# Kernel optimization log

Hardware: AMD Instinct MI355X
Metric: run time of the kernel (lower is better)

The kernel has to match this reference:

```python
import jax, jax.numpy as jnp
import numpy as np
import math

# batch, seq_len, emb_ch, convlru_hidden_ch, spatial H, W (W must equal H, see diag_embed broadcast)
B, L, E, C, H, W = 4, 32, 64, 96, 32, 32


def setup_inputs():
    key = jax.random.key(0)
    ks = jax.random.split(key, 24)
    r_min, r_max = 0.8, 0.99
    u1 = jax.random.uniform(ks[0], (C, H))
    u2 = jax.random.uniform(ks[1], (C, H))
    nu_log = jnp.log(-0.5 * jnp.log(u1 * (r_max ** 2 - r_min ** 2) + r_min ** 2))
    theta_log = jnp.log(u2 * 2.0 * np.pi)
    lam_abs = jnp.exp(-jnp.exp(nu_log))  # |lambda| = exp(-nu)
    gamma_log = jnp.log(jnp.sqrt(1.0 - lam_abs ** 2))
    params_log = jnp.vstack([nu_log, theta_log, gamma_log]).astype(jnp.float32)

    def w(k, shape, fan_in):
        s = 1.0 / np.sqrt(fan_in)
        return jax.random.uniform(k, shape, minval=-s, maxval=s, dtype=jnp.float32)

    return {
        "x": jax.random.normal(ks[2], (B, L, E, H, W), jnp.float32),
        "mask": jnp.ones((B, L), jnp.float32),
        "params_log": params_log,
        "Wb_r": w(ks[3], (C, E), E), "Wb_i": w(ks[4], (C, E), E),
        "bb_r": w(ks[5], (C,), E), "bb_i": w(ks[6], (C,), E),
        "Wp1_r": w(ks[7], (C, C), C), "Wp1_i": w(ks[8], (C, C), C),
        "bp1_r": w(ks[9], (C,), C), "bp1_i": w(ks[10], (C,), C),
        "Wp2_r": w(ks[11], (C, C), C), "Wp2_i": w(ks[12], (C, C), C),
        "bp2_r": w(ks[13], (C,), C), "bp2_i": w(ks[14], (C,), C),
        "Wc_r": w(ks[15], (E, C), C), "Wc_i": w(ks[16], (E, C), C),
        "bc_r": w(ks[17], (E,), C), "bc_i": w(ks[18], (E,), C),
        "ln_w": jnp.ones((E, H, W), jnp.float32),
        "ln_b": jnp.zeros((E, H, W), jnp.float32),
    }


def _forward(x, mask, params_log, Wb, bb, Wp1, bp1, Wp2, bp2, Wc, bc, ln_w, ln_b):
    nu, theta, gamma = jnp.split(jnp.exp(params_log), 3, axis=0)  # each (C, H)
    lamb = jnp.exp(jnp.complex64(-nu + 1j * theta))               # (C, H)
    xc = x.astype(jnp.complex64)
    # proj_B: 1x1 complex conv == channel einsum
    h = jnp.einsum('blehw,ce->blchw', xc, Wb) + bb[:, None, None]
    h = jnp.fft.fft2(h)  # over last two axes
    h = jnp.einsum('blkhw,ck->blchw', h, Wp1) + bp1[:, None, None]
    eye = jnp.eye(H, dtype=jnp.float32)  # (H, W); requires W == H
    # h * torch.diag_embed(gamma): elementwise mult with a diagonal (C,H,H) matrix
    # -> zeroes off-diagonal spatial entries (faithful to the torch code)
    h = h * (gamma[:, :, None] * eye)
    m = jnp.broadcast_to(mask[:, :, None, None, None], h.shape).astype(jnp.float32)
    log2L = int(math.ceil(math.log2(L)))
    lamb = lamb[None]  # (1, C, H)
    for i in range(1, log2L + 1):
        l = 2 ** i
        if i > 1:
            lamb = jnp.concatenate([lamb, lamb * lamb[-1]], axis=0)  # (l//2, C, H)
        hr = h.reshape(B * L // l, l, C, H, W)
        mr = m.reshape(B * L // l, l, C, H, W)
        h1, h2 = hr[:, : l // 2], hr[:, l // 2:]
        # term[n,j,c,a,b] = lamb[j,c,a] * eye[a,b] * h1[n,-1,c,a,b] * mask[n,l//2-1,c,a,b]
        term = (lamb[None, :, :, :, None] * eye) * h1[:, -1:] * mr[:, l // 2 - 1: l // 2]
        h = jnp.concatenate([h1, h2 + term], axis=1).reshape(B, L, C, H, W)
    h = jnp.fft.ifft2(h)
    h = jnp.einsum('blkhw,ck->blchw', h, Wp2) + bp2[:, None, None]
    h = jnp.einsum('blchw,ec->blehw', h, Wc) + bc[:, None, None]
    h = h.real
    # dropout is identity in eval mode
    mu = jnp.mean(h, axis=(-3, -2, -1), keepdims=True)
    var = jnp.var(h, axis=(-3, -2, -1), keepdims=True)
    h = (h - mu) / jnp.sqrt(var + 1e-5) * ln_w + ln_b
    return h + x


def reference(x, mask, params_log, Wb_r, Wb_i, bb_r, bb_i, Wp1_r, Wp1_i, bp1_r, bp1_i, Wp2_r, Wp2_i, bp2_r, bp2_i, Wc_r, Wc_i, bc_r, bc_i, ln_w, ln_b):
    cx = lambda r, i: (r + 1j * i).astype(jnp.complex64)
    return _forward(x, mask, params_log,
                    cx(Wb_r, Wb_i), cx(bb_r, bb_i),
                    cx(Wp1_r, Wp1_i), cx(bp1_r, bp1_i),
                    cx(Wp2_r, Wp2_i), cx(bp2_r, bp2_i),
                    cx(Wc_r, Wc_i), cx(bc_r, bc_i),
                    ln_w, ln_b)
```

## Files before the change

kernel.cpp:

```cpp
#include <hip/hip_runtime.h>

static constexpr int BL = 128;
static constexpr int OFF_COS  = 0;
static constexpr int OFF_SIN  = 1024;
static constexpr int OFF_ARE  = 2048;
static constexpr int OFF_AIM  = 8192;
static constexpr int OFF_WRE  = 14336;
static constexpr int OFF_WIM  = 20480;
static constexpr int OFF_LRE  = 26624;
static constexpr int OFF_LIM  = 29696;
static constexpr int OFF_GAM  = 32768;
static constexpr int OFF_BH0R = 35840;
static constexpr int OFF_BH0I = 35936;
static constexpr int OFF_BRR  = 36032;
static constexpr int OFF_QF   = 36096;
static constexpr int OFF_Y    = 560384;
static constexpr int OFF_V    = 1346816;
static constexpr int OFF_R    = 1871104;
static constexpr int OFF_ST   = 2133248;

__global__ __launch_bounds__(256) void k0_precompute(
    const float* __restrict__ params_log,
    const float* __restrict__ Wb_r, const float* __restrict__ Wb_i,
    const float* __restrict__ bb_r, const float* __restrict__ bb_i,
    const float* __restrict__ Wp1_r, const float* __restrict__ Wp1_i,
    const float* __restrict__ Wp2_r, const float* __restrict__ Wp2_i,
    const float* __restrict__ Wc_r, const float* __restrict__ Wc_i,
    const float* __restrict__ bp2_r, const float* __restrict__ bp2_i,
    const float* __restrict__ bc_r, float* __restrict__ ws) {
  int tid = blockIdx.x * 256 + threadIdx.x;
  if (tid < 1024) {
    int h = tid >> 5, s = tid & 31;
    int m = (h * s) & 31;
    float ang = (float)m * 0.19634954084936207f;
    ws[OFF_COS + tid] = cosf(ang);
    ws[OFF_SIN + tid] = sinf(ang);
  } else if (tid < 4096) {
    int i = tid - 1024;
    float nu = expf(params_log[i]);
    float th = expf(params_log[3072 + i]);
    float g  = expf(params_log[6144 + i]);
    float rr = expf(-nu);
    ws[OFF_LRE + i] = rr * cosf(th);
    ws[OFF_LIM + i] = rr * sinf(th);
    ws[OFF_GAM + i] = g;
  } else if (tid < 10240) {
    int i = tid - 4096;
    int c = i >> 6, e = i & 63;
    float are = 0.f, aim = 0.f;
    for (int k = 0; k < 96; ++k) {
      float pr = Wp1_r[c * 96 + k], pi = Wp1_i[c * 96 + k];
      float wr = Wb_r[k * 64 + e], wi = Wb_i[k * 64 + e];
      are += pr * wr - pi * wi;
      aim += pr * wi + pi * wr;
    }
    ws[OFF_ARE + i] = are;
    ws[OFF_AIM + i] = aim;
  } else if (tid < 16384) {
    int i = tid - 10240;
    int e = i / 96, c = i - e * 96;
    float are = 0.f, aim = 0.f;
    for (int k = 0; k < 96; ++k) {
      float wr = Wc_r[e * 96 + k], wi = Wc_i[e * 96 + k];
      float pr = Wp2_r[k * 96 + c], pi = Wp2_i[k * 96 + c];
      are += wr * pr - wi * pi;
      aim += wr * pi + wi * pr;
    }
    ws[OFF_WRE + i] = are;
    ws[OFF_WIM + i] = aim;
  } else if (tid < 16480) {
    int c = tid - 16384;
    float re = 0.f, im = 0.f;
    for (int k = 0; k < 96; ++k) {
      float pr = Wp1_r[c * 96 + k], pi = Wp1_i[c * 96 + k];
      float br = bb_r[k], bi = bb_i[k];
      re += pr * br - pi * bi;
      im += pr * bi + pi * br;
    }
    ws[OFF_BH0R + c] = 1024.f * re;
    ws[OFF_BH0I + c] = 1024.f * im;
  } else if (tid < 16544) {
    int e = tid - 16480;
    float re = 0.f;
    for (int k = 0; k < 96; ++k)
      re += Wc_r[e * 96 + k] * bp2_r[k] - Wc_i[e * 96 + k] * bp2_i[k];
    ws[OFF_BRR + e] = re + bc_r[e];
  }
}

__global__ __launch_bounds__(256) void k1_qdft(const float* __restrict__ x,
                                               float* __restrict__ ws) {
  __shared__ float pl[4][1024];
  __shared__ float qsh[4][32];
  int wave = threadIdx.x >> 6, lane = threadIdx.x & 63;
  int plane = blockIdx.x * 4 + wave;
  const float* xp = x + (size_t)plane * 1024;
#pragma unroll
  for (int j = 0; j < 16; ++j) pl[wave][j * 64 + lane] = xp[j * 64 + lane];
  __syncthreads();
  int s = lane & 31, half = lane >> 5;
  float acc = 0.f;
#pragma unroll
  for (int u0 = 0; u0 < 16; ++u0) {
    int u = half * 16 + u0;
    acc += pl[wave][u * 32 + ((s - u) & 31)];
  }
  acc += __shfl_xor(acc, 32);
  if (lane < 32) qsh[wave][lane] = acc;
  __syncthreads();
  int h = lane & 31;
  const float* Ft = ws + (lane < 32 ? OFF_COS : OFF_SIN);
  float sum = 0.f;
#pragma unroll
  for (int s2 = 0; s2 < 32; ++s2) sum += qsh[wave][s2] * Ft[s2 * 32 + h];
  if (lane >= 32) sum = -sum;
  ws[OFF_QF + plane * 64 + h * 2 + (lane < 32 ? 0 : 1)] = sum;
}

__global__ __launch_bounds__(256) void k2_mix1(float* __restrict__ ws,
                                               const float* __restrict__ bp1_r,
                                               const float* __restrict__ bp1_i) {
  __shared__ float qre[64][32], qim[64][32];
  int bl = blockIdx.x / 12, chunk = blockIdx.x % 12;
  const float2* qF = (const float2*)(ws + OFF_QF) + bl * 2048;
  for (int i = threadIdx.x; i < 2048; i += 256) {
    float2 v = qF[i];
    qre[i >> 5][i & 31] = v.x;
    qim[i >> 5][i & 31] = v.y;
  }
  __syncthreads();
  int c = chunk * 8 + (threadIdx.x >> 5), h = threadIdx.x & 31;
  const float* Ar = ws + OFF_ARE + c * 64;
  const float* Ai = ws + OFF_AIM + c * 64;
  float re = 0.f, im = 0.f;
#pragma unroll 8
  for (int e = 0; e < 64; ++e) {
    float ar = Ar[e], ai = Ai[e], qr = qre[e][h], qi = qim[e][h];
    re += ar * qr - ai * qi;
    im += ar * qi + ai * qr;
  }
  if (h == 0) { re += ws[OFF_BH0R + c]; im += ws[OFF_BH0I + c]; }
  re += bp1_r[c];
  im += bp1_i[c];
  float g = ws[OFF_GAM + c * 32 + h];
  ((float2*)(ws + OFF_Y))[(bl * 96 + c) * 32 + h] = make_float2(g * re, g * im);
}

__global__ __launch_bounds__(256) void k3_scan(float* __restrict__ ws,
                                               const float* __restrict__ mask) {
  int tid = blockIdx.x * 256 + threadIdx.x;
  int b = tid / 3072, r = tid - b * 3072;
  float lr = ws[OFF_LRE + r], li = ws[OFF_LIM + r];
  float2* Y = (float2*)(ws + OFF_Y) + (size_t)b * 32 * 3072 + r;
  float2 v = Y[0];
  float sr = v.x, si = v.y;
  for (int l = 1; l < 32; ++l) {
    float m = mask[b * 32 + l - 1];
    float cr = m * (lr * sr - li * si);
    float ci = m * (lr * si + li * sr);
    v = Y[l * 3072];
    sr = v.x + cr;
    si = v.y + ci;
    Y[l * 3072] = make_float2(sr, si);
  }
}

__global__ __launch_bounds__(256) void k4_mix2(float* __restrict__ ws) {
  __shared__ float sre[96][32], sim_[96][32];
  int bl = blockIdx.x >> 3, chunk = blockIdx.x & 7;
  const float2* S = (const float2*)(ws + OFF_Y) + bl * 3072;
  for (int i = threadIdx.x; i < 3072; i += 256) {
    float2 v = S[i];
    sre[i >> 5][i & 31] = v.x;
    sim_[i >> 5][i & 31] = v.y;
  }
  __syncthreads();
  int e = chunk * 8 + (threadIdx.x >> 5), h = threadIdx.x & 31;
  const float* Wr = ws + OFF_WRE + e * 96;
  const float* Wi = ws + OFF_WIM + e * 96;
  float re = 0.f, im = 0.f;
#pragma unroll 8
  for (int c = 0; c < 96; ++c) {
    float wr = Wr[c], wi = Wi[c], a = sre[c][h], b2 = sim_[c][h];
    re += wr * a - wi * b2;
    im += wr * b2 + wi * a;
  }
  ((float2*)(ws + OFF_V))[(bl * 64 + e) * 32 + h] = make_float2(re, im);
}

__global__ __launch_bounds__(256) void k5a_post(float* __restrict__ ws) {
  __shared__ float vre[64][32], vim[64][32];
  __shared__ float red[8];
  int bl = blockIdx.x;
  const float2* V = (const float2*)(ws + OFF_V) + bl * 2048;
  for (int i = threadIdx.x; i < 2048; i += 256) {
    float2 v = V[i];
    vre[i >> 5][i & 31] = v.x;
    vim[i >> 5][i & 31] = v.y;
  }
  __syncthreads();
  float sum = 0.f, sumsq = 0.f;
  float* R = ws + OFF_R + bl * 2048;
  for (int i = threadIdx.x; i < 2048; i += 256) {
    int e = i >> 5, s = i & 31;
    float acc = 0.f;
#pragma unroll
    for (int h = 0; h < 32; ++h)
      acc += vre[e][h] * ws[OFF_COS + h * 32 + s] - vim[e][h] * ws[OFF_SIN + h * 32 + s];
    float r = acc * (1.0f / 1024.0f) + ws[OFF_BRR + e];
    R[i] = r;
    sum += r;
    sumsq += r * r;
  }
#pragma unroll
  for (int off = 32; off > 0; off >>= 1) {
    sum += __shfl_down(sum, off);
    sumsq += __shfl_down(sumsq, off);
  }
  int wave = threadIdx.x >> 6, lane = threadIdx.x & 63;
  if (lane == 0) { red[wave] = sum; red[4 + wave] = sumsq; }
  __syncthreads();
  if (threadIdx.x == 0) {
    float s0 = red[0] + red[1] + red[2] + red[3];
    float q0 = red[4] + red[5] + red[6] + red[7];
    float mu = s0 * (1.0f / 2048.0f);
    float var = q0 * (1.0f / 2048.0f) - mu * mu;
    ws[OFF_ST + bl * 2] = mu;
    ws[OFF_ST + bl * 2 + 1] = rsqrtf(var + 1e-5f);
  }
}

__global__ __launch_bounds__(256) void k5b_final(const float* __restrict__ x,
                                                 const float* __restrict__ lnw,
                                                 const float* __restrict__ lnb,
                                                 const float* __restrict__ ws,
                                                 float* __restrict__ out) {
  int gid = blockIdx.x * 256 + threadIdx.x;
  int flat = gid * 4;
  int bl = flat >> 16;
  int rem = flat & 65535;
  int e = rem >> 10;
  int pos = rem & 1023;
  int u = pos >> 5, v = pos & 31;
  float mu = ws[OFF_ST + bl * 2], istd = ws[OFF_ST + bl * 2 + 1];
  const float* Rrow = ws + OFF_R + bl * 2048 + e * 32;
  const float4 xin = ((const float4*)x)[gid];
  const float4 lw = ((const float4*)lnw)[rem >> 2];
  const float4 lb = ((const float4*)lnb)[rem >> 2];
  float4 o;
  o.x = (Rrow[(u + v) & 31] - mu) * istd * lw.x + lb.x + xin.x;
  o.y = (Rrow[(u + v + 1) & 31] - mu) * istd * lw.y + lb.y + xin.y;
  o.z = (Rrow[(u + v + 2) & 31] - mu) * istd * lw.z + lb.z + xin.z;
  o.w = (Rrow[(u + v + 3) & 31] - mu) * istd * lw.w + lb.w + xin.w;
  ((float4*)out)[gid] = o;
}

extern "C" void kernel_launch(void* const* d_in, const int* in_sizes, int n_in,
                              void* d_out, int out_size, void* d_ws, size_t ws_size,
                              hipStream_t stream) {
  const float* x          = (const float*)d_in[0];
  const float* mask       = (const float*)d_in[1];
  const float* params_log = (const float*)d_in[2];
  const float* Wb_r  = (const float*)d_in[3];
  const float* Wb_i  = (const float*)d_in[4];
  const float* bb_r  = (const float*)d_in[5];
  const float* bb_i  = (const float*)d_in[6];
  const float* Wp1_r = (const float*)d_in[7];
  const float* Wp1_i = (const float*)d_in[8];
  const float* bp1_r = (const float*)d_in[9];
  const float* bp1_i = (const float*)d_in[10];
  const float* Wp2_r = (const float*)d_in[11];
  const float* Wp2_i = (const float*)d_in[12];
  const float* bp2_r = (const float*)d_in[13];
  const float* bp2_i = (const float*)d_in[14];
  const float* Wc_r  = (const float*)d_in[15];
  const float* Wc_i  = (const float*)d_in[16];
  const float* bc_r  = (const float*)d_in[17];
  const float* ln_w  = (const float*)d_in[19];
  const float* ln_b  = (const float*)d_in[20];
  float* ws  = (float*)d_ws;
  float* out = (float*)d_out;

  k0_precompute<<<65, 256, 0, stream>>>(params_log, Wb_r, Wb_i, bb_r, bb_i,
                                        Wp1_r, Wp1_i, Wp2_r, Wp2_i, Wc_r, Wc_i,
                                        bp2_r, bp2_i, bc_r, ws);
  k1_qdft<<<2048, 256, 0, stream>>>(x, ws);
  k2_mix1<<<1536, 256, 0, stream>>>(ws, bp1_r, bp1_i);
  k3_scan<<<48, 256, 0, stream>>>(ws, mask);
  k4_mix2<<<1024, 256, 0, stream>>>(ws);
  k5a_post<<<128, 256, 0, stream>>>(ws);
  k5b_final<<<8192, 256, 0, stream>>>(x, ln_w, ln_b, ws, out);
}
```

Measured before the change: 177.3 us.

## Fuse kernels: merge precompute with DFT, mix2 with post, restructure scan

Merges the weight precompute into the spatial DFT kernel as extra blocks, and fuses the output channel mix with the inverse DFT and LayerNorm partial statistics. This cuts the pipeline from seven launches to five and drops the V intermediate. The scan now runs 64-thread blocks that load all 32 timesteps into registers before the recurrence, and the twiddle tables come from a 32-entry in-LDS sincos table instead of global tables. The final kernel stages one R row in shared memory and combines the two partial statistics, at the cost of more register pressure in the scan and the fused mix kernel.

```diff
diff --git a/kernel.cpp b/kernel.cpp
--- a/kernel.cpp
+++ b/kernel.cpp
@@ -15,11 +15,11 @@
 static constexpr int OFF_BRR  = 36032;
 static constexpr int OFF_QF   = 36096;
 static constexpr int OFF_Y    = 560384;
-static constexpr int OFF_V    = 1346816;
 static constexpr int OFF_R    = 1871104;
 static constexpr int OFF_ST   = 2133248;
 
-__global__ __launch_bounds__(256) void k0_precompute(
+__global__ __launch_bounds__(256) void kA(
+    const float* __restrict__ x,
     const float* __restrict__ params_log,
     const float* __restrict__ Wb_r, const float* __restrict__ Wb_i,
     const float* __restrict__ bb_r, const float* __restrict__ bb_i,
@@ -28,106 +28,107 @@
     const float* __restrict__ Wc_r, const float* __restrict__ Wc_i,
     const float* __restrict__ bp2_r, const float* __restrict__ bp2_i,
     const float* __restrict__ bc_r, float* __restrict__ ws) {
-  int tid = blockIdx.x * 256 + threadIdx.x;
-  if (tid < 1024) {
-    int h = tid >> 5, s = tid & 31;
-    int m = (h * s) & 31;
-    float ang = (float)m * 0.19634954084936207f;
-    ws[OFF_COS + tid] = cosf(ang);
-    ws[OFF_SIN + tid] = sinf(ang);
-  } else if (tid < 4096) {
-    int i = tid - 1024;
-    float nu = expf(params_log[i]);
-    float th = expf(params_log[3072 + i]);
-    float g  = expf(params_log[6144 + i]);
-    float rr = expf(-nu);
-    ws[OFF_LRE + i] = rr * cosf(th);
-    ws[OFF_LIM + i] = rr * sinf(th);
-    ws[OFF_GAM + i] = g;
-  } else if (tid < 10240) {
-    int i = tid - 4096;
-    int c = i >> 6, e = i & 63;
-    float are = 0.f, aim = 0.f;
-    for (int k = 0; k < 96; ++k) {
-      float pr = Wp1_r[c * 96 + k], pi = Wp1_i[c * 96 + k];
-      float wr = Wb_r[k * 64 + e], wi = Wb_i[k * 64 + e];
-      are += pr * wr - pi * wi;
-      aim += pr * wi + pi * wr;
-    }
-    ws[OFF_ARE + i] = are;
-    ws[OFF_AIM + i] = aim;
-  } else if (tid < 16384) {
-    int i = tid - 10240;
-    int e = i / 96, c = i - e * 96;
-    float are = 0.f, aim = 0.f;
-    for (int k = 0; k < 96; ++k) {
-      float wr = Wc_r[e * 96 + k], wi = Wc_i[e * 96 + k];
-      float pr = Wp2_r[k * 96 + c], pi = Wp2_i[k * 96 + c];
-      are += wr * pr - wi * pi;
-      aim += wr * pi + wi * pr;
-    }
-    ws[OFF_WRE + i] = are;
-    ws[OFF_WIM + i] = aim;
-  } else if (tid < 16480) {
-    int c = tid - 16384;
-    float re = 0.f, im = 0.f;
-    for (int k = 0; k < 96; ++k) {
-      float pr = Wp1_r[c * 96 + k], pi = Wp1_i[c * 96 + k];
-      float br = bb_r[k], bi = bb_i[k];
-      re += pr * br - pi * bi;
-      im += pr * bi + pi * br;
-    }
-    ws[OFF_BH0R + c] = 1024.f * re;
-    ws[OFF_BH0I + c] = 1024.f * im;
-  } else if (tid < 16544) {
-    int e = tid - 16480;
-    float re = 0.f;
-    for (int k = 0; k < 96; ++k)
-      re += Wc_r[e * 96 + k] * bp2_r[k] - Wc_i[e * 96 + k] * bp2_i[k];
-    ws[OFF_BRR + e] = re + bc_r[e];
-  }
-}
-
-__global__ __launch_bounds__(256) void k1_qdft(const float* __restrict__ x,
-                                               float* __restrict__ ws) {
-  __shared__ float pl[4][1024];
-  __shared__ float qsh[4][32];
-  int wave = threadIdx.x >> 6, lane = threadIdx.x & 63;
-  int plane = blockIdx.x * 4 + wave;
-  const float* xp = x + (size_t)plane * 1024;
-#pragma unroll
-  for (int j = 0; j < 16; ++j) pl[wave][j * 64 + lane] = xp[j * 64 + lane];
-  __syncthreads();
-  int s = lane & 31, half = lane >> 5;
-  float acc = 0.f;
-#pragma unroll
-  for (int u0 = 0; u0 < 16; ++u0) {
-    int u = half * 16 + u0;
-    acc += pl[wave][u * 32 + ((s - u) & 31)];
-  }
-  acc += __shfl_xor(acc, 32);
-  if (lane < 32) qsh[wave][lane] = acc;
-  __syncthreads();
-  int h = lane & 31;
-  const float* Ft = ws + (lane < 32 ? OFF_COS : OFF_SIN);
-  float sum = 0.f;
-#pragma unroll
-  for (int s2 = 0; s2 < 32; ++s2) sum += qsh[wave][s2] * Ft[s2 * 32 + h];
-  if (lane >= 32) sum = -sum;
-  ws[OFF_QF + plane * 64 + h * 2 + (lane < 32 ? 0 : 1)] = sum;
-}
-
-__global__ __launch_bounds__(256) void k2_mix1(float* __restrict__ ws,
-                                               const float* __restrict__ bp1_r,
-                                               const float* __restrict__ bp1_i) {
-  __shared__ float qre[64][32], qim[64][32];
+  if (blockIdx.x < 2048) {
+    __shared__ float pl[4][1024];
+    __shared__ float qsh[4][32];
+    __shared__ float ct[32], st[32];
+    int wave = threadIdx.x >> 6, lane = threadIdx.x & 63;
+    if (threadIdx.x < 32) {
+      float sv, cv;
+      sincosf((float)threadIdx.x * 0.19634954084936207f, &sv, &cv);
+      ct[threadIdx.x] = cv;
+      st[threadIdx.x] = sv;
+    }
+    int plane = blockIdx.x * 4 + wave;
+    const float4* xp = (const float4*)(x + (size_t)plane * 1024);
+    float4* pl4 = (float4*)pl[wave];
+#pragma unroll
+    for (int j = 0; j < 4; ++j) pl4[j * 64 + lane] = xp[j * 64 + lane];
+    __syncthreads();
+    int s = lane & 31, halfw = lane >> 5;
+    float acc = 0.f;
+#pragma unroll
+    for (int u0 = 0; u0 < 16; ++u0) {
+      int u = halfw * 16 + u0;
+      acc += pl[wave][u * 32 + ((s - u) & 31)];
+    }
+    acc += __shfl_xor(acc, 32);
+    if (lane < 32) qsh[wave][lane] = acc;
+    __syncthreads();
+    int h = lane & 31;
+    const float* T = (lane < 32) ? ct : st;
+    float sum = 0.f;
+    int m = 0;
+#pragma unroll
+    for (int s2 = 0; s2 < 32; ++s2) {
+      sum += qsh[wave][s2] * T[m];
+      m = (m + h) & 31;
+    }
+    if (lane >= 32) sum = -sum;
+    ws[OFF_QF + (size_t)plane * 64 + h * 2 + (lane < 32 ? 0 : 1)] = sum;
+  } else {
+    int tid = (int)(blockIdx.x - 2048) * 256 + threadIdx.x;
+    if (tid < 3072) {
+      int i = tid;
+      float nu = expf(params_log[i]);
+      float th = expf(params_log[3072 + i]);
+      float g  = expf(params_log[6144 + i]);
+      float rr = expf(-nu);
+      ws[OFF_LRE + i] = rr * cosf(th);
+      ws[OFF_LIM + i] = rr * sinf(th);
+      ws[OFF_GAM + i] = g;
+    } else if (tid < 9216) {
+      int i = tid - 3072;
+      int c = i >> 6, e = i & 63;
+      float are = 0.f, aim = 0.f;
+      for (int k = 0; k < 96; ++k) {
+        float pr = Wp1_r[c * 96 + k], pi = Wp1_i[c * 96 + k];
+        float wr = Wb_r[k * 64 + e], wi = Wb_i[k * 64 + e];
+        are += pr * wr - pi * wi;
+        aim += pr * wi + pi * wr;
+      }
+      ws[OFF_ARE + i] = are;
+      ws[OFF_AIM + i] = aim;
+    } else if (tid < 15360) {
+      int i = tid - 9216;
+      int e = i / 96, c = i - e * 96;
+      float are = 0.f, aim = 0.f;
+      for (int k = 0; k < 96; ++k) {
+        float wr = Wc_r[e * 96 + k], wi = Wc_i[e * 96 + k];
+        float pr = Wp2_r[k * 96 + c], pi = Wp2_i[k * 96 + c];
+        are += wr * pr - wi * pi;
+        aim += wr * pi + wi * pr;
+      }
+      ws[OFF_WRE + i] = are;
+      ws[OFF_WIM + i] = aim;
+    } else if (tid < 15456) {
+      int c = tid - 15360;
+      float re = 0.f, im = 0.f;
+      for (int k = 0; k < 96; ++k) {
+        float pr = Wp1_r[c * 96 + k], pi = Wp1_i[c * 96 + k];
+        float br = bb_r[k], bi = bb_i[k];
+        re += pr * br - pi * bi;
+        im += pr * bi + pi * br;
+      }
+      ws[OFF_BH0R + c] = 1024.f * re;
+      ws[OFF_BH0I + c] = 1024.f * im;
+    } else if (tid < 15520) {
+      int e = tid - 15456;
+      float re = 0.f;
+      for (int k = 0; k < 96; ++k)
+        re += Wc_r[e * 96 + k] * bp2_r[k] - Wc_i[e * 96 + k] * bp2_i[k];
+      ws[OFF_BRR + e] = re + bc_r[e];
+    }
+  }
+}
+
+__global__ __launch_bounds__(256) void kB(float* __restrict__ ws,
+                                          const float* __restrict__ bp1_r,
+                                          const float* __restrict__ bp1_i) {
+  __shared__ float2 q[64][32];
   int bl = blockIdx.x / 12, chunk = blockIdx.x % 12;
   const float2* qF = (const float2*)(ws + OFF_QF) + bl * 2048;
-  for (int i = threadIdx.x; i < 2048; i += 256) {
-    float2 v = qF[i];
-    qre[i >> 5][i & 31] = v.x;
-    qim[i >> 5][i & 31] = v.y;
-  }
+  for (int i = threadIdx.x; i < 2048; i += 256) q[i >> 5][i & 31] = qF[i];
   __syncthreads();
   int c = chunk * 8 + (threadIdx.x >> 5), h = threadIdx.x & 31;
   const float* Ar = ws + OFF_ARE + c * 64;
@@ -135,9 +136,10 @@
   float re = 0.f, im = 0.f;
 #pragma unroll 8
   for (int e = 0; e < 64; ++e) {
-    float ar = Ar[e], ai = Ai[e], qr = qre[e][h], qi = qim[e][h];
-    re += ar * qr - ai * qi;
-    im += ar * qi + ai * qr;
+    float ar = Ar[e], ai = Ai[e];
+    float2 qv = q[e][h];
+    re += ar * qv.x - ai * qv.y;
+    im += ar * qv.y + ai * qv.x;
   }
   if (h == 0) { re += ws[OFF_BH0R + c]; im += ws[OFF_BH0I + c]; }
   re += bp1_r[c];
@@ -146,69 +148,78 @@
   ((float2*)(ws + OFF_Y))[(bl * 96 + c) * 32 + h] = make_float2(g * re, g * im);
 }
 
-__global__ __launch_bounds__(256) void k3_scan(float* __restrict__ ws,
-                                               const float* __restrict__ mask) {
-  int tid = blockIdx.x * 256 + threadIdx.x;
+__global__ __launch_bounds__(64) void kC(float* __restrict__ ws,
+                                         const float* __restrict__ mask) {
+  int tid = blockIdx.x * 64 + threadIdx.x;
   int b = tid / 3072, r = tid - b * 3072;
   float lr = ws[OFF_LRE + r], li = ws[OFF_LIM + r];
-  float2* Y = (float2*)(ws + OFF_Y) + (size_t)b * 32 * 3072 + r;
-  float2 v = Y[0];
-  float sr = v.x, si = v.y;
+  float2* Y = (float2*)(ws + OFF_Y) + (size_t)b * 3072 * 32 + r;
+  float2 v[32];
+#pragma unroll
+  for (int l = 0; l < 32; ++l) v[l] = Y[(size_t)l * 3072];
+  float sr = v[0].x, si = v[0].y;
+#pragma unroll
   for (int l = 1; l < 32; ++l) {
-    float m = mask[b * 32 + l - 1];
-    float cr = m * (lr * sr - li * si);
-    float ci = m * (lr * si + li * sr);
-    v = Y[l * 3072];
-    sr = v.x + cr;
-    si = v.y + ci;
-    Y[l * 3072] = make_float2(sr, si);
-  }
-}
-
-__global__ __launch_bounds__(256) void k4_mix2(float* __restrict__ ws) {
-  __shared__ float sre[96][32], sim_[96][32];
-  int bl = blockIdx.x >> 3, chunk = blockIdx.x & 7;
-  const float2* S = (const float2*)(ws + OFF_Y) + bl * 3072;
-  for (int i = threadIdx.x; i < 3072; i += 256) {
-    float2 v = S[i];
-    sre[i >> 5][i & 31] = v.x;
-    sim_[i >> 5][i & 31] = v.y;
-  }
-  __syncthreads();
-  int e = chunk * 8 + (threadIdx.x >> 5), h = threadIdx.x & 31;
-  const float* Wr = ws + OFF_WRE + e * 96;
-  const float* Wi = ws + OFF_WIM + e * 96;
-  float re = 0.f, im = 0.f;
-#pragma unroll 8
+    float mk = mask[b * 32 + l - 1];
+    float cr = mk * (lr * sr - li * si);
+    float ci = mk * (lr * si + li * sr);
+    sr = v[l].x + cr;
+    si = v[l].y + ci;
+    v[l] = make_float2(sr, si);
+  }
+#pragma unroll
+  for (int l = 1; l < 32; ++l) Y[(size_t)l * 3072] = v[l];
+}
+
+__global__ __launch_bounds__(256) void kD(float* __restrict__ ws) {
+  __shared__ float2 S[96][32];
+  __shared__ float2 V[32][33];
+  __shared__ float ct[32], st[32];
+  __shared__ float red[8];
+  int bl = blockIdx.x >> 1, half = blockIdx.x & 1;
+  const float2* Sg = (const float2*)(ws + OFF_Y) + bl * 3072;
+  for (int i = threadIdx.x; i < 3072; i += 256) S[i >> 5][i & 31] = Sg[i];
+  if (threadIdx.x < 32) {
+    float sv, cv;
+    sincosf((float)threadIdx.x * 0.19634954084936207f, &sv, &cv);
+    ct[threadIdx.x] = cv;
+    st[threadIdx.x] = sv;
+  }
+  __syncthreads();
+  int h = threadIdx.x & 31, g = threadIdx.x >> 5;
+  float vr[4] = {0.f, 0.f, 0.f, 0.f}, vi[4] = {0.f, 0.f, 0.f, 0.f};
+  int ebase = half * 32 + g;
+#pragma unroll 4
   for (int c = 0; c < 96; ++c) {
-    float wr = Wr[c], wi = Wi[c], a = sre[c][h], b2 = sim_[c][h];
-    re += wr * a - wi * b2;
-    im += wr * b2 + wi * a;
-  }
-  ((float2*)(ws + OFF_V))[(bl * 64 + e) * 32 + h] = make_float2(re, im);
-}
-
-__global__ __launch_bounds__(256) void k5a_post(float* __restrict__ ws) {
-  __shared__ float vre[64][32], vim[64][32];
-  __shared__ float red[8];
-  int bl = blockIdx.x;
-  const float2* V = (const float2*)(ws + OFF_V) + bl * 2048;
-  for (int i = threadIdx.x; i < 2048; i += 256) {
-    float2 v = V[i];
-    vre[i >> 5][i & 31] = v.x;
-    vim[i >> 5][i & 31] = v.y;
-  }
-  __syncthreads();
+    float2 s = S[c][h];
+#pragma unroll
+    for (int k = 0; k < 4; ++k) {
+      int e = ebase + k * 8;
+      float wr = ws[OFF_WRE + e * 96 + c];
+      float wi = ws[OFF_WIM + e * 96 + c];
+      vr[k] += wr * s.x - wi * s.y;
+      vi[k] += wr * s.y + wi * s.x;
+    }
+  }
+#pragma unroll
+  for (int k = 0; k < 4; ++k) V[k * 8 + g][h] = make_float2(vr[k], vi[k]);
+  __syncthreads();
+  float* R = ws + OFF_R + bl * 2048 + half * 1024;
   float sum = 0.f, sumsq = 0.f;
-  float* R = ws + OFF_R + bl * 2048;
-  for (int i = threadIdx.x; i < 2048; i += 256) {
-    int e = i >> 5, s = i & 31;
+#pragma unroll
+  for (int k = 0; k < 4; ++k) {
+    int idx = k * 256 + threadIdx.x;
+    int el = idx >> 5, s2 = idx & 31;
     float acc = 0.f;
-#pragma unroll
-    for (int h = 0; h < 32; ++h)
-      acc += vre[e][h] * ws[OFF_COS + h * 32 + s] - vim[e][h] * ws[OFF_SIN + h * 32 + s];
-    float r = acc * (1.0f / 1024.0f) + ws[OFF_BRR + e];
-    R[i] = r;
+    int m = 0;
+#pragma unroll
+    for (int hh = 0; hh < 32; ++hh) {
+      float2 v = V[el][hh];
+      acc += v.x * ct[m] - v.y * st[m];
+      m = (m + s2) & 31;
+    }
+    float r = acc * (1.0f / 1024.0f) + ws[OFF_BRR + half * 32 + el];
+    R[idx] = r;
     sum += r;
     sumsq += r * r;
   }
@@ -221,37 +232,37 @@
   if (lane == 0) { red[wave] = sum; red[4 + wave] = sumsq; }
   __syncthreads();
   if (threadIdx.x == 0) {
-    float s0 = red[0] + red[1] + red[2] + red[3];
-    float q0 = red[4] + red[5] + red[6] + red[7];
-    float mu = s0 * (1.0f / 2048.0f);
-    float var = q0 * (1.0f / 2048.0f) - mu * mu;
-    ws[OFF_ST + bl * 2] = mu;
-    ws[OFF_ST + bl * 2 + 1] = rsqrtf(var + 1e-5f);
-  }
-}
-
-__global__ __launch_bounds__(256) void k5b_final(const float* __restrict__ x,
-                                                 const float* __restrict__ lnw,
-                                                 const float* __restrict__ lnb,
-                                                 const float* __restrict__ ws,
-                                                 float* __restrict__ out) {
+    ws[OFF_ST + bl * 4 + half * 2]     = red[0] + red[1] + red[2] + red[3];
+    ws[OFF_ST + bl * 4 + half * 2 + 1] = red[4] + red[5] + red[6] + red[7];
+  }
+}
+
+__global__ __launch_bounds__(256) void kE(const float* __restrict__ x,
+                                          const float* __restrict__ lnw,
+                                          const float* __restrict__ lnb,
+                                          const float* __restrict__ ws,
+                                          float* __restrict__ out) {
+  __shared__ float Rs[32];
+  int bl = blockIdx.x >> 6, e = blockIdx.x & 63;
+  if (threadIdx.x < 32)
+    Rs[threadIdx.x] = ws[OFF_R + bl * 2048 + e * 32 + threadIdx.x];
+  const float* stp = ws + OFF_ST + bl * 4;
+  float s0 = stp[0] + stp[2], q0 = stp[1] + stp[3];
+  float mu = s0 * (1.0f / 2048.0f);
+  float istd = rsqrtf(q0 * (1.0f / 2048.0f) - mu * mu + 1e-5f);
+  __syncthreads();
   int gid = blockIdx.x * 256 + threadIdx.x;
-  int flat = gid * 4;
-  int bl = flat >> 16;
-  int rem = flat & 65535;
-  int e = rem >> 10;
-  int pos = rem & 1023;
+  int pos = threadIdx.x * 4;
   int u = pos >> 5, v = pos & 31;
-  float mu = ws[OFF_ST + bl * 2], istd = ws[OFF_ST + bl * 2 + 1];
-  const float* Rrow = ws + OFF_R + bl * 2048 + e * 32;
+  int rem4 = e * 256 + threadIdx.x;
   const float4 xin = ((const float4*)x)[gid];
-  const float4 lw = ((const float4*)lnw)[rem >> 2];
-  const float4 lb = ((const float4*)lnb)[rem >> 2];
+  const float4 lw = ((const float4*)lnw)[rem4];
+  const float4 lb = ((const float4*)lnb)[rem4];
   float4 o;
-  o.x = (Rrow[(u + v) & 31] - mu) * istd * lw.x + lb.x + xin.x;
-  o.y = (Rrow[(u + v + 1) & 31] - mu) * istd * lw.y + lb.y + xin.y;
-  o.z = (Rrow[(u + v + 2) & 31] - mu) * istd * lw.z + lb.z + xin.z;
-  o.w = (Rrow[(u + v + 3) & 31] - mu) * istd * lw.w + lb.w + xin.w;
+  o.x = (Rs[(u + v) & 31] - mu) * istd * lw.x + lb.x + xin.x;
+  o.y = (Rs[(u + v + 1) & 31] - mu) * istd * lw.y + lb.y + xin.y;
+  o.z = (Rs[(u + v + 2) & 31] - mu) * istd * lw.z + lb.z + xin.z;
+  o.w = (Rs[(u + v + 3) & 31] - mu) * istd * lw.w + lb.w + xin.w;
   ((float4*)out)[gid] = o;
 }
 
@@ -281,13 +292,11 @@
   float* ws  = (float*)d_ws;
   float* out = (float*)d_out;
 
-  k0_precompute<<<65, 256, 0, stream>>>(params_log, Wb_r, Wb_i, bb_r, bb_i,
-                                        Wp1_r, Wp1_i, Wp2_r, Wp2_i, Wc_r, Wc_i,
-                                        bp2_r, bp2_i, bc_r, ws);
-  k1_qdft<<<2048, 256, 0, stream>>>(x, ws);
-  k2_mix1<<<1536, 256, 0, stream>>>(ws, bp1_r, bp1_i);
-  k3_scan<<<48, 256, 0, stream>>>(ws, mask);
-  k4_mix2<<<1024, 256, 0, stream>>>(ws);
-  k5a_post<<<128, 256, 0, stream>>>(ws);
-  k5b_final<<<8192, 256, 0, stream>>>(x, ln_w, ln_b, ws, out);
-}
+  kA<<<2109, 256, 0, stream>>>(x, params_log, Wb_r, Wb_i, bb_r, bb_i,
+                               Wp1_r, Wp1_i, Wp2_r, Wp2_i, Wc_r, Wc_i,
+                               bp2_r, bp2_i, bc_r, ws);
+  kB<<<1536, 256, 0, stream>>>(ws, bp1_r, bp1_i);
+  kC<<<192, 64, 0, stream>>>(ws, mask);
+  kD<<<256, 256, 0, stream>>>(ws);
+  kE<<<8192, 256, 0, stream>>>(x, ln_w, ln_b, ws, out);
+}
```

Result: faster. 170.7 us (-3.8%).
